# Kernel tuning notes

Measured on AMD Instinct MI355X. Metric: run time of the kernel, lower is better.

Reference implementation:

```python
import math
import jax, jax.numpy as jnp
import numpy as np

NEG = -1e10


def _rope_cos_sin(T, head_dim, dtype):
    # theta_i = 10000^(-2*(i-1)/dim), i=1..dim/2  ->  j=0..dim/2-1: 10000^(-2j/dim)
    j = jnp.arange(head_dim // 2, dtype=jnp.float32)
    inv_freq = 1.0 / (10000.0 ** (2.0 * j / head_dim))
    t = jnp.arange(T, dtype=jnp.float32)
    ang = t[:, None] * inv_freq[None, :]          # [T, hd/2]
    return jnp.cos(ang).astype(dtype), jnp.sin(ang).astype(dtype)


def _apply_rope(x, cos, sin):
    # x: [B, H, T, hd]; complex multiply (cos + i sin) * (x0 + i x1)
    B, H, T, hd = x.shape
    xr = x.reshape(B, H, T, hd // 2, 2)
    x0, x1 = xr[..., 0], xr[..., 1]
    c = cos[None, None]  # [1,1,T,hd/2]
    s = sin[None, None]
    o0 = c * x0 - s * x1
    o1 = s * x0 + c * x1
    return jnp.stack([o0, o1], axis=-1).reshape(B, H, T, hd)


def setup_inputs() -> dict:
    key = jax.random.key(0)
    ks = jax.random.split(key, 9)
    B, T, C = 2, 2048, 1024
    std = 0.02
    return {
        "x": jax.random.normal(ks[0], (B, T, C), jnp.float32),
        "Wq": jax.random.normal(ks[1], (C, C), jnp.float32) * std,
        "bq": jnp.zeros((C,), jnp.float32),
        "Wk": jax.random.normal(ks[2], (C, C), jnp.float32) * std,
        "bk": jnp.zeros((C,), jnp.float32),
        "Wv": jax.random.normal(ks[3], (C, C), jnp.float32) * std,
        "bv": jnp.zeros((C,), jnp.float32),
        "Wp": jax.random.normal(ks[4], (C, C), jnp.float32) * std,
        "bp": jnp.zeros((C,), jnp.float32),
    }


def reference(x, Wq, bq, Wk, bk, Wv, bv, Wp, bp):
    B, T, C = x.shape
    H = 16
    hd = C // H

    def heads(y):  # [B,T,C] -> [B,H,T,hd]
        return y.reshape(B, T, H, hd).transpose(0, 2, 1, 3)

    q = heads(x @ Wq.T + bq)
    k = heads(x @ Wk.T + bk)
    v = heads(x @ Wv.T + bv)

    cos, sin = _rope_cos_sin(T, hd, x.dtype)
    q = _apply_rope(q, cos, sin)
    k = _apply_rope(k, cos, sin)

    att = jnp.einsum('bhqd,bhkd->bhqk', q, k) * (1.0 / math.sqrt(hd))
    causal = jnp.tril(jnp.ones((T, T), bool))
    att = jnp.where(causal[None, None], att, jnp.asarray(NEG, att.dtype))
    att = jax.nn.softmax(att, axis=-1)

    y = jnp.einsum('bhqk,bhkd->bhqd', att, v)
    y = y.transpose(0, 2, 1, 3).reshape(B, T, C)
    return y @ Wp.T + bp
```

## Files before the change

### kernel.cpp

```cpp
#include <hip/hip_runtime.h>
#include <math.h>

typedef unsigned short u16;
typedef unsigned int u32;
typedef unsigned long long u64;
typedef __attribute__((ext_vector_type(8))) short short8;
typedef __attribute__((ext_vector_type(4))) short short4v;
typedef __attribute__((ext_vector_type(4))) float f32x4;
typedef __attribute__((ext_vector_type(4))) u16 u16x4;
typedef __attribute__((ext_vector_type(2))) u32 u32x2;
typedef __attribute__((ext_vector_type(4))) u32 u32x4;

#define AS1 __attribute__((address_space(1)))
#define AS3 __attribute__((address_space(3)))

#define QSCALE 0.18033688011112042f

__device__ __forceinline__ u16 f2bf(float f) {
  union { float f; u32 i; } u; u.f = f;
  u32 r = u.i + 0x7FFFu + ((u.i >> 16) & 1u);
  return (u16)(r >> 16);
}

__device__ __forceinline__ u32 pk_bf16(float a, float b) {
  u32 r;
  asm volatile("v_cvt_pk_bf16_f32 %0, %1, %2" : "=v"(r) : "v"(a), "v"(b));
  return r;
}

__device__ __forceinline__ void gl_lds16(const void* g, void* l) {
  __builtin_amdgcn_global_load_lds((const AS1 u32*)g, (AS3 u32*)l, 16, 0, 0);
}

#define MFMA32(a, b, c) __builtin_amdgcn_mfma_f32_16x16x32_bf16(a, b, c, 0, 0, 0)

__device__ __forceinline__ f32x4 mfma16(short4v a, short4v b, f32x4 c) {
#if __has_builtin(__builtin_amdgcn_mfma_f32_16x16x16_bf16)
  return __builtin_amdgcn_mfma_f32_16x16x16_bf16(a, b, c, 0, 0, 0);
#elif __has_builtin(__builtin_amdgcn_mfma_f32_16x16x16bf16_1k)
  return __builtin_amdgcn_mfma_f32_16x16x16bf16_1k(a, b, c, 0, 0, 0);
#else
  f32x4 d = c;
  asm("v_mfma_f32_16x16x16_bf16 %0, %1, %2, %0" : "+v"(d) : "v"(a), "v"(b));
  return d;
#endif
}

__global__ void cvt_all(const float* __restrict__ x,
                        const float* __restrict__ Wq, const float* __restrict__ Wk,
                        const float* __restrict__ Wv, const float* __restrict__ Wp,
                        u16* __restrict__ xb,
                        u16* __restrict__ Wqb, u16* __restrict__ Wkb,
                        u16* __restrict__ Wvb, u16* __restrict__ Wpb,
                        float* __restrict__ cosT, float* __restrict__ sinT,
                        int n4x, int nhalf) {
  int i = blockIdx.x * 256 + threadIdx.x;
  if (i >= nhalf) {
    int k = i - nhalf;
    int t = k >> 5, j = k & 31;
    float inv = powf(10000.0f, -(float)j / 32.0f);
    float ang = (float)t * inv;
    cosT[k] = cosf(ang);
    sinT[k] = sinf(ang);
    return;
  }
  const int i2 = i * 2;
  const float* src; u16* dst; int off;
  if (i2 < n4x) { src = x; dst = xb; off = i2; }
  else {
    int wi = i2 - n4x;
    int sel = wi >> 18;
    off = wi & ((1 << 18) - 1);
    src = sel == 0 ? Wq : sel == 1 ? Wk : sel == 2 ? Wv : Wp;
    dst = sel == 0 ? Wqb : sel == 1 ? Wkb : sel == 2 ? Wvb : Wpb;
  }
  float4 v0 = ((const float4*)src)[off];
  float4 v1 = ((const float4*)src)[off + 1];
  u16x4 o0 = { f2bf(v0.x), f2bf(v0.y), f2bf(v0.z), f2bf(v0.w) };
  u16x4 o1 = { f2bf(v1.x), f2bf(v1.y), f2bf(v1.z), f2bf(v1.w) };
  ((u16x4*)dst)[off] = o0;
  ((u16x4*)dst)[off + 1] = o1;
}

__global__ __launch_bounds__(256, 3) void gemm_qkv(
    const u16* __restrict__ xb,
    const u16* __restrict__ Wqb, const u16* __restrict__ Wkb, const u16* __restrict__ Wvb,
    const float* __restrict__ bq, const float* __restrict__ bk, const float* __restrict__ bv,
    const float* __restrict__ cosT, const float* __restrict__ sinT,
    u16* __restrict__ Qb, u16* __restrict__ Kb, u16* __restrict__ Vb) {
  const int K = 1024, N = 1024;
  __shared__ __attribute__((aligned(16))) u16 As[128 * 64];
  __shared__ __attribute__((aligned(16))) u16 Bs[128 * 64];
  const int tid = threadIdx.x;
  const int lane = tid & 63;
  const int hi = lane >> 4, cc = lane & 15;
  const int w = tid >> 6, wm = w >> 1, wn = w & 1;

  const int lin = blockIdx.x + 24 * blockIdx.y;
  const int a_ = lin & 7;
  const int m_ = lin >> 3;
  const int c_ = a_ * 3 + (m_ % 3);
  const int sel = c_ >> 3;
  const int row0 = (m_ / 3) * 128, col0 = (c_ & 7) * 128;

  const u16* W = sel == 0 ? Wqb : sel == 1 ? Wkb : Wvb;
  const float* bias = sel == 0 ? bq : sel == 1 ? bk : bv;
  u16* Out = sel == 0 ? Qb : sel == 1 ? Kb : Vb;

  const int lr = tid >> 3;
  const int lkb = (((tid & 7) ^ (lr & 7)) * 8);
  const u16* Ag = xb + (size_t)(row0 + lr) * K + lkb;
  const u16* Wg = W + (size_t)(col0 + lr) * K + lkb;

  f32x4 acc[4][4];
#pragma unroll
  for (int m = 0; m < 4; ++m)
#pragma unroll
    for (int n = 0; n < 4; ++n) acc[m][n] = f32x4{0.f, 0.f, 0.f, 0.f};

  for (int k0 = 0; k0 < K; k0 += 64) {
    __syncthreads();
#pragma unroll
    for (int j = 0; j < 4; ++j) {
      gl_lds16(Ag + (size_t)j * 32 * K + k0, As + j * 2048 + tid * 8);
      gl_lds16(Wg + (size_t)j * 32 * K + k0, Bs + j * 2048 + tid * 8);
    }
    __syncthreads();
    short8 a[2][4], b[2][4];
#pragma unroll
    for (int kk = 0; kk < 2; ++kk) {
#pragma unroll
      for (int m = 0; m < 4; ++m)
        a[kk][m] = *(const short8*)(As + (wm * 64 + m * 16 + cc) * 64 +
                                    (((kk * 4 + hi) ^ (cc & 7)) * 8));
#pragma unroll
      for (int n = 0; n < 4; ++n)
        b[kk][n] = *(const short8*)(Bs + (wn * 64 + n * 16 + cc) * 64 +
                                    (((kk * 4 + hi) ^ (cc & 7)) * 8));
    }
#pragma unroll
    for (int kk = 0; kk < 2; ++kk)
#pragma unroll
      for (int m = 0; m < 4; ++m)
#pragma unroll
        for (int n = 0; n < 4; ++n)
          acc[m][n] = MFMA32(a[kk][m], b[kk][n], acc[m][n]);
  }

  if (sel < 2) {
    const float qs = (sel == 0) ? QSCALE : 1.0f;
#pragma unroll
    for (int n = 0; n < 4; ++n) {
      const int col = col0 + wn * 64 + n * 16 + cc;
      const int j = (col & 63) >> 1;
      const float bb = bias[col];
#pragma unroll
      for (int m = 0; m < 4; ++m) {
        const int rw = row0 + wm * 64 + m * 16 + hi * 4;
#pragma unroll
        for (int r = 0; r < 4; ++r) {
          const int row = rw + r;
          const int t = row & 2047;
          float v = acc[m][n][r] + bb;
          float pv = __shfl_xor(v, 1);
          float c = cosT[t * 32 + j], s = sinT[t * 32 + j];
          float oo = (cc & 1) ? (s * pv + c * v) : (c * v - s * pv);
          Out[(size_t)row * N + col] = f2bf(oo * qs);
        }
      }
    }
  } else {
#pragma unroll
    for (int n = 0; n < 4; ++n) {
      const int col = col0 + wn * 64 + n * 16 + cc;
      const float bb = bias[col];
#pragma unroll
      for (int m = 0; m < 4; ++m) {
        const int rw = row0 + wm * 64 + m * 16 + hi * 4;
#pragma unroll
        for (int r = 0; r < 4; ++r)
          Out[(size_t)(rw + r) * N + col] = f2bf(acc[m][n][r] + bb);
      }
    }
  }
}

__global__ __launch_bounds__(512, 3) void flash_mfma(
    const u16* __restrict__ Qb, const u16* __restrict__ Kb,
    const u16* __restrict__ Vb, u16* __restrict__ Yb) {
  const int T = 2048, C = 1024;
  __shared__ __attribute__((aligned(16))) u16 Ks[64 * 64];
  __shared__ __attribute__((aligned(16))) u16 Vt[64 * 64];

  const int tid = threadIdx.x;
  const int lane = tid & 63;
  const int hi = lane >> 4, cc = lane & 15;
  const int hi4 = hi * 4;
  const int w = tid >> 6;
  const int wl = w & 3;
  const int isB = w >> 2;

  const int lin = blockIdx.x + 16 * blockIdx.y;
  const int bh  = (lin & 7) * 4 + ((lin >> 3) & 3);
  const int qtA = lin >> 5;
  const int qtB = 31 - qtA;
  const int qtW = isB ? qtB : qtA;
  const size_t hbase = (size_t)(bh >> 4) * T * C + (size_t)(bh & 15) * 64;
  const int q0w = qtW * 64 + wl * 16;

  short8 qa0, qa1;
  {
    const u16* qp = Qb + hbase + (size_t)(q0w + cc) * C + hi * 8;
    qa0 = *(const short8*)qp;
    qa1 = *(const short8*)(qp + 32);
  }

  f32x4 o[4];
#pragma unroll
  for (int dc = 0; dc < 4; ++dc) o[dc] = f32x4{0.f, 0.f, 0.f, 0.f};
  float mrow = -1e30f, lsum = 0.f;

  const int krow = tid >> 3, kcol = (tid & 7) * 8;
  const int vd0 = (tid & 31) * 2, vkey0 = (tid >> 5) * 4;
  const int g = tid >> 5;
  const int sb = (g & 3) * 16 + (g >> 2) * 4;
  const u16* kgp = Kb + hbase + (size_t)krow * C + kcol;
  const u16* vgp = Vb + hbase + (size_t)vkey0 * C + vd0;

  short8 kr0;
  u32 vr_[4];

  auto LOADT = [&](int kt) {
    const size_t off = (size_t)(kt * 64) * C;
    kr0 = *(const short8*)(kgp + off);
#pragma unroll
    for (int j = 0; j < 4; ++j)
      vr_[j] = *(const u32*)(vgp + off + (size_t)j * C);
  };

  char* KsB = (char*)Ks;
  char* VtB = (char*)Vt;

  auto WRITET = [&]() {
    const int kb = krow * 128 + kcol * 2;
    const int ksw = (krow & 7) << 4;
    *(short8*)(KsB + (kb ^ ksw)) = kr0;
    u32 lo0 = (vr_[0] & 0xFFFFu) | (vr_[1] << 16);
    u32 lo1 = (vr_[2] & 0xFFFFu) | (vr_[3] << 16);
    u32 hh0 = (vr_[0] >> 16) | (vr_[1] & 0xFFFF0000u);
    u32 hh1 = (vr_[2] >> 16) | (vr_[3] & 0xFFFF0000u);
    const int d1 = vd0 + 1;
    u32x2 vlo = {lo0, lo1};
    u32x2 vhi = {hh0, hh1};
    *(u32x2*)(VtB + ((vd0 * 128 + sb * 2) ^ ((vd0 & 7) << 4))) = vlo;
    *(u32x2*)(VtB + ((d1 * 128 + sb * 2) ^ ((d1 & 7) << 4))) = vhi;
  };

  const int ksw2 = (cc & 7) << 4;

  LOADT(0);
  WRITET();
  LOADT(1);
  __syncthreads();

  for (int kt = 0; kt <= qtB; ++kt) {
    const bool act = (kt <= qtW);
    if (act) {
      f32x4 s[4];
#pragma unroll
      for (int nt = 0; nt < 4; ++nt) {
        const int kb = (nt * 16 + cc) * 128 + hi * 16;
        short8 kf0 = *(const short8*)(KsB + (kb ^ ksw2));
        short8 kf1 = *(const short8*)(KsB + ((kb + 64) ^ ksw2));
        f32x4 z = f32x4{0.f, 0.f, 0.f, 0.f};
        z = MFMA32(kf0, qa0, z);
        z = MFMA32(kf1, qa1, z);
        s[nt] = z;
      }

      if (kt == qtW) {
        const int qloc = wl * 16 + cc;
#pragma unroll
        for (int nt = 0; nt < 4; ++nt)
#pragma unroll
          for (int r = 0; r < 4; ++r)
            if (nt * 16 + hi4 + r > qloc) s[nt][r] = -1e30f;
      }

      float tm = s[0][0];
#pragma unroll
      for (int nt = 0; nt < 4; ++nt)
#pragma unroll
        for (int r = 0; r < 4; ++r) tm = fmaxf(tm, s[nt][r]);
      tm = fmaxf(tm, __shfl_xor(tm, 16));
      tm = fmaxf(tm, __shfl_xor(tm, 32));
      const bool need = tm > mrow + 8.0f;
      float corr = 1.0f;
      if (need) { corr = exp2f(mrow - tm); mrow = tm; }

      short4v pa[4];
      float psum = 0.f;
#pragma unroll
      for (int nt = 0; nt < 4; ++nt) {
        float e0 = exp2f(s[nt][0] - mrow);
        float e1 = exp2f(s[nt][1] - mrow);
        float e2 = exp2f(s[nt][2] - mrow);
        float e3 = exp2f(s[nt][3] - mrow);
        psum += (e0 + e1) + (e2 + e3);
        union { u32 u[2]; short4v v; } pu;
        pu.u[0] = pk_bf16(e0, e1);
        pu.u[1] = pk_bf16(e2, e3);
        pa[nt] = pu.v;
      }
      psum += __shfl_xor(psum, 16);
      psum += __shfl_xor(psum, 32);
      lsum = lsum * corr + psum;

      if (__any(need)) {
        f32x4 cv;
        cv[0] = __shfl(corr, hi4 + 0);
        cv[1] = __shfl(corr, hi4 + 1);
        cv[2] = __shfl(corr, hi4 + 2);
        cv[3] = __shfl(corr, hi4 + 3);
#pragma unroll
        for (int dc = 0; dc < 4; ++dc) o[dc] *= cv;
      }

#pragma unroll
      for (int np = 0; np < 2; ++np)
#pragma unroll
        for (int dc = 0; dc < 4; ++dc) {
          short8 vb2 = *(const short8*)(VtB + (((dc * 16 + cc) * 128 + hi * 32 + np * 16) ^ ksw2));
          short4v vlo = __builtin_shufflevector(vb2, vb2, 0, 1, 2, 3);
          short4v vhi = __builtin_shufflevector(vb2, vb2, 4, 5, 6, 7);
          o[dc] = mfma16(pa[2 * np], vlo, o[dc]);
          o[dc] = mfma16(pa[2 * np + 1], vhi, o[dc]);
        }
    }

    if (kt < qtB) {
      __syncthreads();
      WRITET();
      if (kt + 1 < qtB) LOADT(kt + 2);
      __syncthreads();
    }
  }

  f32x4 iv;
  iv[0] = 1.0f / __shfl(lsum, hi4 + 0);
  iv[1] = 1.0f / __shfl(lsum, hi4 + 1);
  iv[2] = 1.0f / __shfl(lsum, hi4 + 2);
  iv[3] = 1.0f / __shfl(lsum, hi4 + 3);
#pragma unroll
  for (int dc = 0; dc < 4; ++dc)
#pragma unroll
    for (int r = 0; r < 4; ++r)
      Yb[hbase + (size_t)(q0w + hi4 + r) * C + dc * 16 + cc] = f2bf(o[dc][r] * iv[r]);
}

__global__ __launch_bounds__(256, 2) void gemm_proj(
    const u16* __restrict__ A, const u16* __restrict__ W,
    const float* __restrict__ bias, float* __restrict__ Out) {
  const int K = 1024, N = 1024;
  __shared__ __attribute__((aligned(16))) u16 As[128 * 64];
  __shared__ __attribute__((aligned(16))) u16 Bs[64 * 64];
  const int tid = threadIdx.x;
  const int lane = tid & 63;
  const int hi = lane >> 4, cc = lane & 15;
  const int w = tid >> 6, wm = w >> 1, wn = w & 1;

  const int lin = blockIdx.x + 16 * blockIdx.y;
  const int colt = (lin & 7) * 2 + ((lin >> 3) & 1);
  const int row0 = (lin >> 4) * 128, col0 = colt * 64;

  const int lr = tid >> 3;
  const int lkb = (((tid & 7) ^ (lr & 7)) * 8);
  const u16* Ag = A + (size_t)(row0 + lr) * K + lkb;
  const u16* Wg = W + (size_t)(col0 + lr) * K + lkb;

  f32x4 acc[4][2];
#pragma unroll
  for (int m = 0; m < 4; ++m)
#pragma unroll
    for (int n = 0; n < 2; ++n) acc[m][n] = f32x4{0.f, 0.f, 0.f, 0.f};

  for (int k0 = 0; k0 < K; k0 += 64) {
    __syncthreads();
#pragma unroll
    for (int j = 0; j < 4; ++j)
      gl_lds16(Ag + (size_t)j * 32 * K + k0, As + j * 2048 + tid * 8);
#pragma unroll
    for (int j = 0; j < 2; ++j)
      gl_lds16(Wg + (size_t)j * 32 * K + k0, Bs + j * 2048 + tid * 8);
    __syncthreads();
    short8 a[2][4], b[2][2];
#pragma unroll
    for (int kk = 0; kk < 2; ++kk) {
#pragma unroll
      for (int m = 0; m < 4; ++m)
        a[kk][m] = *(const short8*)(As + (wm * 64 + m * 16 + cc) * 64 +
                                    (((kk * 4 + hi) ^ (cc & 7)) * 8));
#pragma unroll
      for (int n = 0; n < 2; ++n)
        b[kk][n] = *(const short8*)(Bs + (wn * 32 + n * 16 + cc) * 64 +
                                    (((kk * 4 + hi) ^ (cc & 7)) * 8));
    }
#pragma unroll
    for (int kk = 0; kk < 2; ++kk)
#pragma unroll
      for (int m = 0; m < 4; ++m)
#pragma unroll
        for (int n = 0; n < 2; ++n)
          acc[m][n] = MFMA32(a[kk][m], b[kk][n], acc[m][n]);
  }

#pragma unroll
  for (int n = 0; n < 2; ++n) {
    const int col = col0 + wn * 32 + n * 16 + cc;
    const float bb = bias[col];
#pragma unroll
    for (int m = 0; m < 4; ++m) {
      const int rw = row0 + wm * 64 + m * 16 + hi * 4;
#pragma unroll
      for (int r = 0; r < 4; ++r)
        Out[(size_t)(rw + r) * N + col] = acc[m][n][r] + bb;
    }
  }
}

extern "C" void kernel_launch(void* const* d_in, const int* in_sizes, int n_in,
                              void* d_out, int out_size, void* d_ws, size_t ws_size,
                              hipStream_t stream) {
  const float* x  = (const float*)d_in[0];
  const float* Wq = (const float*)d_in[1];
  const float* bq = (const float*)d_in[2];
  const float* Wk = (const float*)d_in[3];
  const float* bk = (const float*)d_in[4];
  const float* Wv = (const float*)d_in[5];
  const float* bv = (const float*)d_in[6];
  const float* Wp = (const float*)d_in[7];
  const float* bp = (const float*)d_in[8];
  float* out = (float*)d_out;

  const int B = 2, T = 2048, C = 1024;
  const int M = B * T;
  const size_t MC = (size_t)M * C;
  const size_t CC = (size_t)C * C;

  char* p = (char*)d_ws;
  u16* xb  = (u16*)p;  p += MC * 2;
  u16* Wqb = (u16*)p;  p += CC * 2;
  u16* Wkb = (u16*)p;  p += CC * 2;
  u16* Wvb = (u16*)p;  p += CC * 2;
  u16* Wpb = (u16*)p;  p += CC * 2;
  u16* Qbb = (u16*)p;  p += MC * 2;
  u16* Kbb = (u16*)p;  p += MC * 2;
  u16* Vbb = (u16*)p;  p += MC * 2;
  float* cosT = (float*)p; p += (size_t)T * 32 * 4;
  float* sinT = (float*)p; p += (size_t)T * 32 * 4;

  const int n4x = (int)(MC / 4);
  const int n4tot = n4x + 4 * (int)(CC / 4);
  const int nhalf = n4tot / 2;
  const int ntot = nhalf + T * 32;
  cvt_all<<<(ntot + 255) / 256, 256, 0, stream>>>(x, Wq, Wk, Wv, Wp,
                                                  xb, Wqb, Wkb, Wvb, Wpb,
                                                  cosT, sinT, n4x, nhalf);

  dim3 gq(24, M / 128);
  gemm_qkv<<<gq, 256, 0, stream>>>(xb, Wqb, Wkb, Wvb, bq, bk, bv, cosT, sinT, Qbb, Kbb, Vbb);

  dim3 fg(16, B * 16);
  flash_mfma<<<fg, 512, 0, stream>>>(Qbb, Kbb, Vbb, xb);

  dim3 gp(C / 64, M / 128);
  gemm_proj<<<gp, 256, 0, stream>>>(xb, Wpb, bp, out);
}
```

Baseline: 113.6 us.

## Convert weights to bf16 inside GEMM tile loads; add MFMA priority hints in attention

Weights are no longer converted to bf16 by a separate pass. The QKV and projection GEMMs now read fp32 weights with register loads, pack them to bf16 and store them into shared memory. This drops the weight write and re-read through a workspace buffer, but each GEMM tile now loads twice the bytes of weight data and loses the async global-to-LDS path for the B operand. Separately, s_setprio is raised around the MFMA sections of the flash-attention loop so waves in their matrix phase get scheduling priority.

```diff
diff --git a/kernel.cpp b/kernel.cpp
--- a/kernel.cpp
+++ b/kernel.cpp
@@ -46,14 +46,18 @@
 #endif
 }
 
-__global__ void cvt_all(const float* __restrict__ x,
-                        const float* __restrict__ Wq, const float* __restrict__ Wk,
-                        const float* __restrict__ Wv, const float* __restrict__ Wp,
-                        u16* __restrict__ xb,
-                        u16* __restrict__ Wqb, u16* __restrict__ Wkb,
-                        u16* __restrict__ Wvb, u16* __restrict__ Wpb,
+__device__ __forceinline__ u32x4 pk8(const float4& a, const float4& b) {
+  u32x4 r;
+  r[0] = pk_bf16(a.x, a.y);
+  r[1] = pk_bf16(a.z, a.w);
+  r[2] = pk_bf16(b.x, b.y);
+  r[3] = pk_bf16(b.z, b.w);
+  return r;
+}
+
+__global__ void cvt_all(const float* __restrict__ x, u16* __restrict__ xb,
                         float* __restrict__ cosT, float* __restrict__ sinT,
-                        int n4x, int nhalf) {
+                        int nhalf) {
   int i = blockIdx.x * 256 + threadIdx.x;
   if (i >= nhalf) {
     int k = i - nhalf;
@@ -64,27 +68,18 @@
     sinT[k] = sinf(ang);
     return;
   }
-  const int i2 = i * 2;
-  const float* src; u16* dst; int off;
-  if (i2 < n4x) { src = x; dst = xb; off = i2; }
-  else {
-    int wi = i2 - n4x;
-    int sel = wi >> 18;
-    off = wi & ((1 << 18) - 1);
-    src = sel == 0 ? Wq : sel == 1 ? Wk : sel == 2 ? Wv : Wp;
-    dst = sel == 0 ? Wqb : sel == 1 ? Wkb : sel == 2 ? Wvb : Wpb;
-  }
-  float4 v0 = ((const float4*)src)[off];
-  float4 v1 = ((const float4*)src)[off + 1];
+  const int off = i * 2;
+  float4 v0 = ((const float4*)x)[off];
+  float4 v1 = ((const float4*)x)[off + 1];
   u16x4 o0 = { f2bf(v0.x), f2bf(v0.y), f2bf(v0.z), f2bf(v0.w) };
   u16x4 o1 = { f2bf(v1.x), f2bf(v1.y), f2bf(v1.z), f2bf(v1.w) };
-  ((u16x4*)dst)[off] = o0;
-  ((u16x4*)dst)[off + 1] = o1;
+  ((u16x4*)xb)[off] = o0;
+  ((u16x4*)xb)[off + 1] = o1;
 }
 
 __global__ __launch_bounds__(256, 3) void gemm_qkv(
     const u16* __restrict__ xb,
-    const u16* __restrict__ Wqb, const u16* __restrict__ Wkb, const u16* __restrict__ Wvb,
+    const float* __restrict__ Wq32, const float* __restrict__ Wk32, const float* __restrict__ Wv32,
     const float* __restrict__ bq, const float* __restrict__ bk, const float* __restrict__ bv,
     const float* __restrict__ cosT, const float* __restrict__ sinT,
     u16* __restrict__ Qb, u16* __restrict__ Kb, u16* __restrict__ Vb) {
@@ -103,14 +98,14 @@
   const int sel = c_ >> 3;
   const int row0 = (m_ / 3) * 128, col0 = (c_ & 7) * 128;
 
-  const u16* W = sel == 0 ? Wqb : sel == 1 ? Wkb : Wvb;
+  const float* W32 = sel == 0 ? Wq32 : sel == 1 ? Wk32 : Wv32;
   const float* bias = sel == 0 ? bq : sel == 1 ? bk : bv;
   u16* Out = sel == 0 ? Qb : sel == 1 ? Kb : Vb;
 
   const int lr = tid >> 3;
   const int lkb = (((tid & 7) ^ (lr & 7)) * 8);
   const u16* Ag = xb + (size_t)(row0 + lr) * K + lkb;
-  const u16* Wg = W + (size_t)(col0 + lr) * K + lkb;
+  const float* Wg = W32 + (size_t)(col0 + lr) * K + lkb;
 
   f32x4 acc[4][4];
 #pragma unroll
@@ -119,12 +114,20 @@
     for (int n = 0; n < 4; ++n) acc[m][n] = f32x4{0.f, 0.f, 0.f, 0.f};
 
   for (int k0 = 0; k0 < K; k0 += 64) {
+    float4 wa[4], wb[4];
+#pragma unroll
+    for (int j = 0; j < 4; ++j) {
+      const float* src = Wg + (size_t)j * 32 * K + k0;
+      wa[j] = *(const float4*)src;
+      wb[j] = *(const float4*)(src + 4);
+    }
     __syncthreads();
 #pragma unroll
-    for (int j = 0; j < 4; ++j) {
+    for (int j = 0; j < 4; ++j)
       gl_lds16(Ag + (size_t)j * 32 * K + k0, As + j * 2048 + tid * 8);
-      gl_lds16(Wg + (size_t)j * 32 * K + k0, Bs + j * 2048 + tid * 8);
-    }
+#pragma unroll
+    for (int j = 0; j < 4; ++j)
+      *(u32x4*)(Bs + j * 2048 + tid * 8) = pk8(wa[j], wb[j]);
     __syncthreads();
     short8 a[2][4], b[2][4];
 #pragma unroll
@@ -267,6 +270,7 @@
     const bool act = (kt <= qtW);
     if (act) {
       f32x4 s[4];
+      __builtin_amdgcn_s_setprio(1);
 #pragma unroll
       for (int nt = 0; nt < 4; ++nt) {
         const int kb = (nt * 16 + cc) * 128 + hi * 16;
@@ -277,6 +281,7 @@
         z = MFMA32(kf1, qa1, z);
         s[nt] = z;
       }
+      __builtin_amdgcn_s_setprio(0);
 
       if (kt == qtW) {
         const int qloc = wl * 16 + cc;
@@ -326,6 +331,7 @@
         for (int dc = 0; dc < 4; ++dc) o[dc] *= cv;
       }
 
+      __builtin_amdgcn_s_setprio(1);
 #pragma unroll
       for (int np = 0; np < 2; ++np)
 #pragma unroll
@@ -336,6 +342,7 @@
           o[dc] = mfma16(pa[2 * np], vlo, o[dc]);
           o[dc] = mfma16(pa[2 * np + 1], vhi, o[dc]);
         }
+      __builtin_amdgcn_s_setprio(0);
     }
 
     if (kt < qtB) {
@@ -359,7 +366,7 @@
 }
 
 __global__ __launch_bounds__(256, 2) void gemm_proj(
-    const u16* __restrict__ A, const u16* __restrict__ W,
+    const u16* __restrict__ A, const float* __restrict__ W32,
     const float* __restrict__ bias, float* __restrict__ Out) {
   const int K = 1024, N = 1024;
   __shared__ __attribute__((aligned(16))) u16 As[128 * 64];
@@ -376,7 +383,7 @@
   const int lr = tid >> 3;
   const int lkb = (((tid & 7) ^ (lr & 7)) * 8);
   const u16* Ag = A + (size_t)(row0 + lr) * K + lkb;
-  const u16* Wg = W + (size_t)(col0 + lr) * K + lkb;
+  const float* Wg = W32 + (size_t)(col0 + lr) * K + lkb;
 
   f32x4 acc[4][2];
 #pragma unroll
@@ -385,13 +392,20 @@
     for (int n = 0; n < 2; ++n) acc[m][n] = f32x4{0.f, 0.f, 0.f, 0.f};
 
   for (int k0 = 0; k0 < K; k0 += 64) {
+    float4 wa[2], wb[2];
+#pragma unroll
+    for (int j = 0; j < 2; ++j) {
+      const float* src = Wg + (size_t)j * 32 * K + k0;
+      wa[j] = *(const float4*)src;
+      wb[j] = *(const float4*)(src + 4);
+    }
     __syncthreads();
 #pragma unroll
     for (int j = 0; j < 4; ++j)
       gl_lds16(Ag + (size_t)j * 32 * K + k0, As + j * 2048 + tid * 8);
 #pragma unroll
     for (int j = 0; j < 2; ++j)
-      gl_lds16(Wg + (size_t)j * 32 * K + k0, Bs + j * 2048 + tid * 8);
+      *(u32x4*)(Bs + j * 2048 + tid * 8) = pk8(wa[j], wb[j]);
     __syncthreads();
     short8 a[2][4], b[2][2];
 #pragma unroll
@@ -445,34 +459,25 @@
   const int B = 2, T = 2048, C = 1024;
   const int M = B * T;
   const size_t MC = (size_t)M * C;
-  const size_t CC = (size_t)C * C;
 
   char* p = (char*)d_ws;
   u16* xb  = (u16*)p;  p += MC * 2;
-  u16* Wqb = (u16*)p;  p += CC * 2;
-  u16* Wkb = (u16*)p;  p += CC * 2;
-  u16* Wvb = (u16*)p;  p += CC * 2;
-  u16* Wpb = (u16*)p;  p += CC * 2;
   u16* Qbb = (u16*)p;  p += MC * 2;
   u16* Kbb = (u16*)p;  p += MC * 2;
   u16* Vbb = (u16*)p;  p += MC * 2;
   float* cosT = (float*)p; p += (size_t)T * 32 * 4;
   float* sinT = (float*)p; p += (size_t)T * 32 * 4;
 
-  const int n4x = (int)(MC / 4);
-  const int n4tot = n4x + 4 * (int)(CC / 4);
-  const int nhalf = n4tot / 2;
+  const int nhalf = (int)(MC / 8);
   const int ntot = nhalf + T * 32;
-  cvt_all<<<(ntot + 255) / 256, 256, 0, stream>>>(x, Wq, Wk, Wv, Wp,
-                                                  xb, Wqb, Wkb, Wvb, Wpb,
-                                                  cosT, sinT, n4x, nhalf);
+  cvt_all<<<(ntot + 255) / 256, 256, 0, stream>>>(x, xb, cosT, sinT, nhalf);
 
   dim3 gq(24, M / 128);
-  gemm_qkv<<<gq, 256, 0, stream>>>(xb, Wqb, Wkb, Wvb, bq, bk, bv, cosT, sinT, Qbb, Kbb, Vbb);
+  gemm_qkv<<<gq, 256, 0, stream>>>(xb, Wq, Wk, Wv, bq, bk, bv, cosT, sinT, Qbb, Kbb, Vbb);
 
   dim3 fg(16, B * 16);
   flash_mfma<<<fg, 512, 0, stream>>>(Qbb, Kbb, Vbb, xb);
 
   dim3 gp(C / 64, M / 128);
-  gemm_proj<<<gp, 256, 0, stream>>>(xb, Wpb, bp, out);
-}
+  gemm_proj<<<gp, 256, 0, stream>>>(xb, Wp, bp, out);
+}
```

Measured after the change: 118.7 us. 1.04x slower.
